# Kernel tuning notes

Hardware: AMD Instinct MI355X
Metric: run time of the kernel (lower is better)

## Reference

```python
import jax, jax.numpy as jnp
import numpy as np

B, REP = 32, 1024
N_VERBS, N_ROLES, N_NOUNS, MR = 504, 190, 11538, 6
HID, NHEADS, MAXN = 32, 4, 512


def setup_inputs() -> dict:
    key = jax.random.key(0)
    ks = jax.random.split(key, 16)
    s = 0.05  # weight scale
    return {
        "rep": jax.random.normal(ks[0], (B, REP), jnp.float32),
        "W_v": jax.random.normal(ks[1], (REP, N_VERBS), jnp.float32) * s,
        "b_v": jax.random.normal(ks[2], (N_VERBS,), jnp.float32) * s,
        "W_r": jax.random.normal(ks[3], (REP, N_ROLES * HID), jnp.float32) * s,
        "b_r": jax.random.normal(ks[4], (N_ROLES * HID,), jnp.float32) * s,
        "attn_in_w": jax.random.normal(ks[5], (3, 3 * HID, HID), jnp.float32) * s,
        "attn_in_b": jax.random.normal(ks[6], (3, 3 * HID), jnp.float32) * s,
        "attn_out_w": jax.random.normal(ks[7], (3, HID, HID), jnp.float32) * s,
        "attn_out_b": jax.random.normal(ks[8], (3, HID), jnp.float32) * s,
        "W_n": jax.random.normal(ks[9], (HID, N_NOUNS), jnp.float32) * s,
        "b_n": jax.random.normal(ks[10], (N_NOUNS,), jnp.float32) * s,
        "r_n_idx": jax.random.randint(ks[11], (N_ROLES, MAXN), 0, N_NOUNS, jnp.int32),
        "pad_v_r": jax.random.randint(ks[12], (N_VERBS, MR), 0, N_ROLES + 1, jnp.int32),
    }


def _mha(x, in_w, in_b, out_w, out_b):
    # x: [L, B, E] self-attention, torch nn.MultiheadAttention semantics
    L, Bn, E = x.shape
    hd = E // NHEADS
    qkv = x @ in_w.T + in_b                      # [L, B, 3E]
    q, k, v = jnp.split(qkv, 3, axis=-1)
    q = q.reshape(L, Bn, NHEADS, hd)
    k = k.reshape(L, Bn, NHEADS, hd)
    v = v.reshape(L, Bn, NHEADS, hd)
    scores = jnp.einsum("lbhd,mbhd->bhlm", q, k) / jnp.sqrt(jnp.float32(hd))
    attn = jax.nn.softmax(scores, axis=-1)
    out = jnp.einsum("bhlm,mbhd->lbhd", attn, v).reshape(L, Bn, E)
    return out @ out_w.T + out_b


def reference(rep, W_v, b_v, W_r, b_r, attn_in_w, attn_in_b, attn_out_w,
              attn_out_b, W_n, b_n, r_n_idx, pad_v_r):
    batch = rep.shape[0]
    v_potential = rep @ W_v + b_v                          # [B, V]
    node = (rep @ W_r + b_r).reshape(batch, N_ROLES, HID)
    node = jnp.transpose(node, (1, 0, 2))                  # [R, B, H]
    for i in range(3):
        node = _mha(node, attn_in_w[i], attn_in_b[i], attn_out_w[i], attn_out_b[i])
    rn_potential = node @ W_n + b_n                        # [R, B, N_nouns]

    # grouped index_select per role: [R, B, MAXN]
    grouped = jax.vmap(lambda pot, idx: pot[:, idx])(rn_potential, r_n_idx)
    r_max = grouped.max(axis=-1)                           # [R, B]
    maxi = grouped.argmax(axis=-1)                         # [R, B]
    rn_marginal = r_max + jnp.log(jnp.exp(grouped - r_max[..., None]).sum(-1))
    r_maxi = jax.vmap(lambda idx, mi: idx[mi])(r_n_idx, maxi)  # global noun ids

    # [B, R] then prepend the zero/padding column -> [B, 1+R]
    zeros_f = jnp.zeros((batch, 1), rn_marginal.dtype)
    zeros_i = jnp.zeros((batch, 1), r_maxi.dtype)
    rn_marginal = jnp.concatenate([zeros_f, rn_marginal.T], axis=1)
    r_max = jnp.concatenate([zeros_f, r_max.T], axis=1)
    r_maxi = jnp.concatenate([zeros_i, r_maxi.T], axis=1)

    # gather per-verb role groups: [B, V, MR]
    vrn_marginal_g = rn_marginal[:, pad_v_r]
    vr_max_g = r_max[:, pad_v_r]
    vr_maxi_g = r_maxi[:, pad_v_r]

    v_marginal = vrn_marginal_g.sum(2) + v_potential       # [B, V]
    m = v_marginal.max(1)
    norm = m + jnp.log(jnp.exp(v_marginal - m[:, None]).sum(1))
    v_max = vr_max_g.sum(2) + v_potential                  # [B, V]
    return (rep, v_potential, rn_potential, norm, v_max, vr_maxi_g)
```

## Files before the change

### kernel.cpp

```cpp
#include <hip/hip_runtime.h>
#include <math.h>

#define B_    32
#define REP_  1024
#define NV_   504
#define NR_   190
#define NN_   11538
#define MR_   6
#define HID_  32
#define NH_   4
#define HD_   8
#define MAXN_ 512

#define O_VP   32768
#define O_RN   48896
#define O_NORM 70199936
#define O_VMAX 70199968
#define O_MAXI 70216096

#define W_REPT  0
#define W_WT    32768
#define W_PN    401984
#define W_PV    1958464
#define W_N0    2087488
#define W_HOB   2282048
#define W_HOA   2476608
#define W_MARG  2671168
#define W_RMAX  2677248
#define W_RMAXI 2683328
#define W_WC    2689408

__global__ __launch_bounds__(256) void k_tr_rep(const float* __restrict__ rep,
                                                float* __restrict__ repT) {
    int gid = blockIdx.x * 256 + threadIdx.x;
    int b = gid & 31, k = gid >> 5;
    repT[gid] = rep[b * REP_ + k];
}

__global__ __launch_bounds__(256) void k_pre(const float* __restrict__ Wn,
                                             float* __restrict__ Wt,
                                             const float* __restrict__ ainw,
                                             const float* __restrict__ ainb,
                                             const float* __restrict__ aoutw,
                                             const float* __restrict__ aoutb,
                                             float* __restrict__ wc) {
    __shared__ float t[32][33];
    int tid = threadIdx.x;
    if (blockIdx.x < 361) {
        int n0 = blockIdx.x * 32;
        #pragma unroll
        for (int p = 0; p < 4; p++) {
            int idx = p * 256 + tid;
            int k = idx >> 5, n = idx & 31;
            int nn = n0 + n;
            t[k][n] = (nn < NN_) ? Wn[(size_t)k * NN_ + nn] : 0.f;
        }
        __syncthreads();
        #pragma unroll
        for (int p = 0; p < 4; p++) {
            int idx = p * 256 + tid;
            int n = idx >> 5, k = idx & 31;
            int nn = n0 + n;
            if (nn < NN_) Wt[nn * 32 + k] = t[k][n];
        }
    } else {
        #pragma unroll 1
        for (int layer = 0; layer < 2; layer++) {
            const float* iw  = ainw + (layer + 1) * 3072;
            const float* ib  = ainb + (layer + 1) * 96;
            const float* ow  = aoutw + layer * 1024;
            const float* obv = aoutb + layer * 32;
            float* W = wc + layer * 3168;
            for (int idx = tid; idx < 3072; idx += 256) {
                int row = idx >> 5, d = idx & 31;
                float s = 0.f;
                #pragma unroll
                for (int e = 0; e < 32; e++) s += iw[row * 32 + e] * ow[e * 32 + d];
                W[idx] = s;
            }
            if (tid < 96) {
                float s = ib[tid];
                #pragma unroll
                for (int e = 0; e < 32; e++) s += iw[tid * 32 + e] * obv[e];
                W[3072 + tid] = s;
            }
        }
    }
}

__global__ __launch_bounds__(256) void k_gemm(const float* __restrict__ Wr,
                                              const float* __restrict__ Wv,
                                              const float4* __restrict__ repT4,
                                              float* __restrict__ pn,
                                              float* __restrict__ pv) {
    int bx = blockIdx.x;
    int lane = threadIdx.x & 63;
    int bg = threadIdx.x >> 6;
    int k0 = blockIdx.y * 128;
    int rbase = k0 * 8 + bg * 2;
    float acc[8] = {0.f,0.f,0.f,0.f,0.f,0.f,0.f,0.f};
    if (bx < 95) {
        int c = bx * 64 + lane;
        const float* w = Wr + (size_t)k0 * 6080 + c;
        #pragma unroll 4
        for (int k = 0; k < 128; k++) {
            float wv = w[(size_t)k * 6080];
            float4 ra = repT4[rbase + k * 8];
            float4 rb = repT4[rbase + k * 8 + 1];
            acc[0] += ra.x * wv; acc[1] += ra.y * wv; acc[2] += ra.z * wv; acc[3] += ra.w * wv;
            acc[4] += rb.x * wv; acc[5] += rb.y * wv; acc[6] += rb.z * wv; acc[7] += rb.w * wv;
        }
        size_t base = (size_t)blockIdx.y * 194560 + (size_t)(bg * 8) * 6080 + c;
        #pragma unroll
        for (int i = 0; i < 8; i++) pn[base + (size_t)i * 6080] = acc[i];
    } else {
        int c = (bx - 95) * 64 + lane;
        if (c >= NV_) return;
        const float* w = Wv + (size_t)k0 * NV_ + c;
        #pragma unroll 4
        for (int k = 0; k < 128; k++) {
            float wv = w[(size_t)k * NV_];
            float4 ra = repT4[rbase + k * 8];
            float4 rb = repT4[rbase + k * 8 + 1];
            acc[0] += ra.x * wv; acc[1] += ra.y * wv; acc[2] += ra.z * wv; acc[3] += ra.w * wv;
            acc[4] += rb.x * wv; acc[5] += rb.y * wv; acc[6] += rb.z * wv; acc[7] += rb.w * wv;
        }
        size_t base = (size_t)blockIdx.y * 16128 + (size_t)(bg * 8) * NV_ + c;
        #pragma unroll
        for (int i = 0; i < 8; i++) pv[base + (size_t)i * NV_] = acc[i];
    }
}

__global__ __launch_bounds__(256) void k_reduce(const float* __restrict__ pn,
                                                const float* __restrict__ pv,
                                                const float* __restrict__ br,
                                                const float* __restrict__ bv,
                                                float* __restrict__ node0,
                                                float* __restrict__ vpot) {
    int bid = blockIdx.x, tid = threadIdx.x;
    if (bid < 760) {
        int gid = bid * 256 + tid;
        int b = gid / 6080, c = gid - b * 6080;
        float s = br[c];
        #pragma unroll
        for (int kz = 0; kz < 8; kz++) s += pn[kz * 194560 + gid];
        node0[(c >> 5) * 1024 + b * 32 + (c & 31)] = s;
    } else {
        int gid = (bid - 760) * 256 + tid;
        int v = gid % NV_;
        float s = bv[v];
        #pragma unroll
        for (int kz = 0; kz < 8; kz++) s += pv[kz * 16128 + gid];
        vpot[gid] = s;
    }
}

__global__ __launch_bounds__(256) void k_attn(const float* __restrict__ xin,
                                              const float* __restrict__ winw,
                                              const float* __restrict__ winb,
                                              float* __restrict__ ho) {
    int b = blockIdx.x >> 2, h = blockIdx.x & 3;
    int tid = threadIdx.x;
    __shared__ __align__(16) float qs[192 * 12];
    __shared__ __align__(16) float ks[192 * 12];
    __shared__ __align__(16) float vs[192 * 12];
    __shared__ __align__(16) float pmS[4 * 192];
    __shared__ __align__(16) float psS[4 * 192];
    __shared__ __align__(16) float poS[4 * 192 * 8];

    if (tid < NR_) {
        const float* xr = xin + tid * 1024 + b * 32;
        float4 xv[8];
        #pragma unroll
        for (int q = 0; q < 8; q++) xv[q] = *(const float4*)(xr + q * 4);
        #pragma unroll 1
        for (int part = 0; part < 3; part++) {
            float* dst = (part == 0) ? qs : (part == 1) ? ks : vs;
            #pragma unroll 1
            for (int jj = 0; jj < 8; jj++) {
                int row = part * 32 + h * 8 + jj;
                const float* wr = winw + row * 32;
                float s = winb[row];
                #pragma unroll
                for (int q = 0; q < 8; q++) {
                    s += xv[q].x * wr[q*4+0] + xv[q].y * wr[q*4+1] +
                         xv[q].z * wr[q*4+2] + xv[q].w * wr[q*4+3];
                }
                dst[tid * 12 + jj] = s;
            }
        }
    }
    __syncthreads();

    int wave = tid >> 6, lane = tid & 63;
    int m0 = wave * 48;
    int m1 = (m0 + 48 < NR_) ? (m0 + 48) : NR_;
    float4 qa[3], qb[3];
    #pragma unroll
    for (int i = 0; i < 3; i++) {
        int l = lane + 64 * i;
        if (l < NR_) {
            qa[i] = *(const float4*)&qs[l * 12];
            qb[i] = *(const float4*)&qs[l * 12 + 4];
        } else {
            qa[i] = make_float4(0.f,0.f,0.f,0.f);
            qb[i] = make_float4(0.f,0.f,0.f,0.f);
        }
    }
    float mM[3] = {-INFINITY, -INFINITY, -INFINITY};
    float sS[3] = {0.f, 0.f, 0.f};
    float o[3][8];
    #pragma unroll
    for (int i = 0; i < 3; i++)
        #pragma unroll
        for (int d = 0; d < 8; d++) o[i][d] = 0.f;
    const float scale = 0.3535533905932738f;
    for (int mm = m0; mm < m1; mm++) {
        float4 ka = *(const float4*)&ks[mm * 12];
        float4 kb = *(const float4*)&ks[mm * 12 + 4];
        float4 va = *(const float4*)&vs[mm * 12];
        float4 vb = *(const float4*)&vs[mm * 12 + 4];
        #pragma unroll
        for (int i = 0; i < 3; i++) {
            float sc = (qa[i].x*ka.x + qa[i].y*ka.y + qa[i].z*ka.z + qa[i].w*ka.w +
                        qb[i].x*kb.x + qb[i].y*kb.y + qb[i].z*kb.z + qb[i].w*kb.w) * scale;
            if (sc > mM[i]) {
                float al = __expf(mM[i] - sc);
                sS[i] = sS[i] * al + 1.f;
                mM[i] = sc;
                o[i][0] = o[i][0]*al + va.x; o[i][1] = o[i][1]*al + va.y;
                o[i][2] = o[i][2]*al + va.z; o[i][3] = o[i][3]*al + va.w;
                o[i][4] = o[i][4]*al + vb.x; o[i][5] = o[i][5]*al + vb.y;
                o[i][6] = o[i][6]*al + vb.z; o[i][7] = o[i][7]*al + vb.w;
            } else {
                float p = __expf(sc - mM[i]);
                sS[i] += p;
                o[i][0] += p*va.x; o[i][1] += p*va.y; o[i][2] += p*va.z; o[i][3] += p*va.w;
                o[i][4] += p*vb.x; o[i][5] += p*vb.y; o[i][6] += p*vb.z; o[i][7] += p*vb.w;
            }
        }
    }
    #pragma unroll
    for (int i = 0; i < 3; i++) {
        int slot = wave * 192 + lane + 64 * i;
        pmS[slot] = mM[i];
        psS[slot] = sS[i];
        *(float4*)&poS[slot * 8]     = make_float4(o[i][0], o[i][1], o[i][2], o[i][3]);
        *(float4*)&poS[slot * 8 + 4] = make_float4(o[i][4], o[i][5], o[i][6], o[i][7]);
    }
    __syncthreads();

    if (tid < NR_) {
        float M = pmS[tid], S = psS[tid];
        float4 oa = *(const float4*)&poS[tid * 8];
        float4 ob = *(const float4*)&poS[tid * 8 + 4];
        #pragma unroll
        for (int w = 1; w < 4; w++) {
            int slot = w * 192 + tid;
            float m2 = pmS[slot], s2 = psS[slot];
            float4 pa = *(const float4*)&poS[slot * 8];
            float4 pb = *(const float4*)&poS[slot * 8 + 4];
            if (m2 > M) {
                float al = __expf(M - m2);
                S = S * al + s2;
                oa.x = oa.x*al + pa.x; oa.y = oa.y*al + pa.y; oa.z = oa.z*al + pa.z; oa.w = oa.w*al + pa.w;
                ob.x = ob.x*al + pb.x; ob.y = ob.y*al + pb.y; ob.z = ob.z*al + pb.z; ob.w = ob.w*al + pb.w;
                M = m2;
            } else {
                float p = __expf(m2 - M);
                S += s2 * p;
                oa.x += p*pa.x; oa.y += p*pa.y; oa.z += p*pa.z; oa.w += p*pa.w;
                ob.x += p*pb.x; ob.y += p*pb.y; ob.z += p*pb.z; ob.w += p*pb.w;
            }
        }
        float inv = 1.f / S;
        float* hp = ho + tid * 1024 + b * 32 + h * 8;
        *(float4*)hp       = make_float4(oa.x*inv, oa.y*inv, oa.z*inv, oa.w*inv);
        *(float4*)(hp + 4) = make_float4(ob.x*inv, ob.y*inv, ob.z*inv, ob.w*inv);
    }
}

__global__ __launch_bounds__(256) void k_big(const float* __restrict__ ho3,
                                             const float* __restrict__ ow3,
                                             const float* __restrict__ ob3,
                                             const float* __restrict__ Wn,
                                             const float* __restrict__ bn,
                                             const float* __restrict__ Wt,
                                             const int* __restrict__ rni,
                                             float* __restrict__ out_rn,
                                             float* __restrict__ marg,
                                             float* __restrict__ rmax,
                                             int* __restrict__ rmaxi) {
    int l = blockIdx.x;
    int tid = threadIdx.x;
    __shared__ float owT[1024];
    __shared__ float As[1024];
    __shared__ float pm[32 * 8], psum[32 * 8];
    __shared__ int   pj[32 * 8];

    for (int i = tid; i < 1024; i += 256) {
        int d = i >> 5, hh = i & 31;
        owT[i] = ow3[hh * 32 + d];
    }

    if (blockIdx.y < 23) {
        int b = tid >> 3, hq = tid & 7;
        float4 hv[8];
        {
            const float4* hp = (const float4*)&ho3[(size_t)l * 1024 + b * 32];
            #pragma unroll
            for (int q = 0; q < 8; q++) hv[q] = hp[q];
        }
        __syncthreads();
        {
            float4 a = *(const float4*)&ob3[hq * 4];
            #pragma unroll
            for (int dq = 0; dq < 8; dq++) {
                float4 h4 = hv[dq];
                float4 w0 = *(const float4*)&owT[(dq*4+0)*32 + hq*4];
                float4 w1 = *(const float4*)&owT[(dq*4+1)*32 + hq*4];
                float4 w2 = *(const float4*)&owT[(dq*4+2)*32 + hq*4];
                float4 w3 = *(const float4*)&owT[(dq*4+3)*32 + hq*4];
                a.x += h4.x*w0.x + h4.y*w1.x + h4.z*w2.x + h4.w*w3.x;
                a.y += h4.x*w0.y + h4.y*w1.y + h4.z*w2.y + h4.w*w3.y;
                a.z += h4.x*w0.z + h4.y*w1.z + h4.z*w2.z + h4.w*w3.z;
                a.w += h4.x*w0.w + h4.y*w1.w + h4.z*w2.w + h4.w*w3.w;
            }
            *(float4*)&As[b * 32 + hq * 4] = a;
        }
        __syncthreads();

        int t0 = l * 32;
        int c0 = blockIdx.y * 512;
        int wave = tid >> 6, lane = tid & 63;
        int r0 = wave * 8;
        int c = c0 + lane * 8;
        int rem = NN_ - c;
        if (rem <= 0) return;
        if (rem >= 8) {
            float acc[8][8];
            #pragma unroll
            for (int r = 0; r < 8; r++)
                #pragma unroll
                for (int q = 0; q < 8; q++) acc[r][q] = 0.f;
            #pragma unroll 1
            for (int g = 0; g < 8; g++) {
                float4 av[8];
                #pragma unroll
                for (int r = 0; r < 8; r++)
                    av[r] = *(const float4*)&As[(r0 + r) * 32 + g * 4];
                #pragma unroll
                for (int kk = 0; kk < 4; kk++) {
                    int k = g * 4 + kk;
                    const float* wp = &Wn[(size_t)k * NN_ + c];
                    float2 w0 = *(const float2*)(wp);
                    float2 w1 = *(const float2*)(wp + 2);
                    float2 w2 = *(const float2*)(wp + 4);
                    float2 w3 = *(const float2*)(wp + 6);
                    #pragma unroll
                    for (int r = 0; r < 8; r++) {
                        float a = ((const float*)&av[r])[kk];
                        acc[r][0] += a * w0.x; acc[r][1] += a * w0.y;
                        acc[r][2] += a * w1.x; acc[r][3] += a * w1.y;
                        acc[r][4] += a * w2.x; acc[r][5] += a * w2.y;
                        acc[r][6] += a * w3.x; acc[r][7] += a * w3.y;
                    }
                }
            }
            float bb[8];
            #pragma unroll
            for (int q = 0; q < 8; q++) bb[q] = bn[c + q];
            #pragma unroll
            for (int r = 0; r < 8; r++) {
                size_t base = (size_t)(t0 + r0 + r) * NN_ + c;
                float v0 = acc[r][0]+bb[0], v1 = acc[r][1]+bb[1];
                float v2 = acc[r][2]+bb[2], v3 = acc[r][3]+bb[3];
                float v4 = acc[r][4]+bb[4], v5 = acc[r][5]+bb[5];
                float v6 = acc[r][6]+bb[6], v7 = acc[r][7]+bb[7];
                if (((r0 + r) & 1) == 0) {
                    *(float4*)&out_rn[base]     = make_float4(v0, v1, v2, v3);
                    *(float4*)&out_rn[base + 4] = make_float4(v4, v5, v6, v7);
                } else {
                    *(float2*)&out_rn[base]     = make_float2(v0, v1);
                    *(float4*)&out_rn[base + 2] = make_float4(v2, v3, v4, v5);
                    *(float2*)&out_rn[base + 6] = make_float2(v6, v7);
                }
            }
        } else {
            for (int e = 0; e < rem; e++) {
                float acc[8] = {0.f,0.f,0.f,0.f,0.f,0.f,0.f,0.f};
                for (int k = 0; k < 32; k++) {
                    float wv = Wn[(size_t)k * NN_ + c + e];
                    #pragma unroll
                    for (int r = 0; r < 8; r++) acc[r] += As[(r0 + r) * 32 + k] * wv;
                }
                float bv2 = bn[c + e];
                #pragma unroll
                for (int r = 0; r < 8; r++)
                    out_rn[(size_t)(t0 + r0 + r) * NN_ + c + e] = acc[r] + bv2;
            }
        }
    } else {
        int jg = tid >> 5, b = tid & 31;
        float4 hv[8];
        {
            const float4* hp = (const float4*)&ho3[(size_t)l * 1024 + b * 32];
            #pragma unroll
            for (int q = 0; q < 8; q++) hv[q] = hp[q];
        }
        __syncthreads();
        float4 nd[8];
        #pragma unroll
        for (int q = 0; q < 8; q++) {
            float4 a = *(const float4*)&ob3[q * 4];
            #pragma unroll
            for (int dq = 0; dq < 8; dq++) {
                float4 h4 = hv[dq];
                float4 w0 = *(const float4*)&owT[(dq*4+0)*32 + q*4];
                float4 w1 = *(const float4*)&owT[(dq*4+1)*32 + q*4];
                float4 w2 = *(const float4*)&owT[(dq*4+2)*32 + q*4];
                float4 w3 = *(const float4*)&owT[(dq*4+3)*32 + q*4];
                a.x += h4.x*w0.x + h4.y*w1.x + h4.z*w2.x + h4.w*w3.x;
                a.y += h4.x*w0.y + h4.y*w1.y + h4.z*w2.y + h4.w*w3.y;
                a.z += h4.x*w0.z + h4.y*w1.z + h4.z*w2.z + h4.w*w3.z;
                a.w += h4.x*w0.w + h4.y*w1.w + h4.z*w2.w + h4.w*w3.w;
            }
            nd[q] = a;
        }
        float lm = -INFINITY, ls = 0.f;
        int jm = 0;
        const int* ip = &rni[l * 512];
        for (int jj = 0; jj < 64; jj++) {
            int j = jg * 64 + jj;
            int idx = ip[j];
            const float4* wr = (const float4*)&Wt[idx * 32];
            float s = bn[idx];
            #pragma unroll
            for (int q = 0; q < 8; q++) {
                float4 w4 = wr[q];
                s += nd[q].x*w4.x + nd[q].y*w4.y + nd[q].z*w4.z + nd[q].w*w4.w;
            }
            if (s > lm) { ls = ls * __expf(lm - s) + 1.f; lm = s; jm = j; }
            else        { ls += __expf(s - lm); }
        }
        pm[b * 8 + jg] = lm; psum[b * 8 + jg] = ls; pj[b * 8 + jg] = jm;
        __syncthreads();
        if (tid < 32) {
            int bb = tid;
            float M = pm[bb * 8], S = psum[bb * 8];
            int J = pj[bb * 8];
            for (int i = 1; i < 8; i++) {
                float m2 = pm[bb * 8 + i], s2 = psum[bb * 8 + i];
                if (m2 > M) { S = S * __expf(M - m2) + s2; M = m2; J = pj[bb * 8 + i]; }
                else        { S += s2 * __expf(m2 - M); }
            }
            int t = l * 32 + bb;
            marg[t]  = M + logf(S);
            rmax[t]  = M;
            rmaxi[t] = ip[J];
        }
    }
}

__global__ __launch_bounds__(256) void k_final(const float* __restrict__ marg,
                                               const float* __restrict__ rmax,
                                               const int* __restrict__ rmaxi,
                                               const int* __restrict__ pad,
                                               const float* __restrict__ vpot,
                                               float* __restrict__ out_norm,
                                               float* __restrict__ out_vmax,
                                               float* __restrict__ out_maxi) {
    int b = blockIdx.x, tid = threadIdx.x;
    __shared__ float me[191], xe[191];
    __shared__ int ie[191];
    __shared__ float vm[NV_];
    __shared__ float rbuf[4];
    if (tid < 191) {
        if (tid == 0) { me[0] = 0.f; xe[0] = 0.f; ie[0] = 0; }
        else {
            int t = (tid - 1) * 32 + b;
            me[tid] = marg[t]; xe[tid] = rmax[t]; ie[tid] = rmaxi[t];
        }
    }
    __syncthreads();
    for (int v = tid; v < NV_; v += 256) {
        float sm = 0.f, sx = 0.f;
        float vp = vpot[b * NV_ + v];
        #pragma unroll
        for (int i = 0; i < 6; i++) {
            int p = pad[v * 6 + i];
            sm += me[p]; sx += xe[p];
            out_maxi[(size_t)(b * NV_ + v) * 6 + i] = (float)ie[p];
        }
        vm[v] = sm + vp;
        out_vmax[b * NV_ + v] = sx + vp;
    }
    __syncthreads();
    float m = -INFINITY;
    for (int v = tid; v < NV_; v += 256) m = fmaxf(m, vm[v]);
    #pragma unroll
    for (int off = 32; off > 0; off >>= 1) m = fmaxf(m, __shfl_xor(m, off));
    if ((tid & 63) == 0) rbuf[tid >> 6] = m;
    __syncthreads();
    float M = fmaxf(fmaxf(rbuf[0], rbuf[1]), fmaxf(rbuf[2], rbuf[3]));
    __syncthreads();
    float s = 0.f;
    for (int v = tid; v < NV_; v += 256) s += __expf(vm[v] - M);
    #pragma unroll
    for (int off = 32; off > 0; off >>= 1) s += __shfl_xor(s, off);
    if ((tid & 63) == 0) rbuf[tid >> 6] = s;
    __syncthreads();
    if (tid == 0) out_norm[b] = M + logf(rbuf[0] + rbuf[1] + rbuf[2] + rbuf[3]);
}

extern "C" void kernel_launch(void* const* d_in, const int* in_sizes, int n_in,
                              void* d_out, int out_size, void* d_ws, size_t ws_size,
                              hipStream_t stream) {
    const float* rep   = (const float*)d_in[0];
    const float* Wv    = (const float*)d_in[1];
    const float* bv    = (const float*)d_in[2];
    const float* Wr    = (const float*)d_in[3];
    const float* br    = (const float*)d_in[4];
    const float* ainw  = (const float*)d_in[5];
    const float* ainb  = (const float*)d_in[6];
    const float* aoutw = (const float*)d_in[7];
    const float* aoutb = (const float*)d_in[8];
    const float* Wn    = (const float*)d_in[9];
    const float* bn    = (const float*)d_in[10];
    const int*   rni   = (const int*)d_in[11];
    const int*   pad   = (const int*)d_in[12];
    float* out = (float*)d_out;
    float* ws  = (float*)d_ws;

    float* repT = ws + W_REPT;
    float* Wt   = ws + W_WT;
    float* pn   = ws + W_PN;
    float* pv   = ws + W_PV;
    float* n0   = ws + W_N0;
    float* hoA  = ws + W_HOA;
    float* hoB  = ws + W_HOB;
    float* marg = ws + W_MARG;
    float* rmx  = ws + W_RMAX;
    int*   rmi  = (int*)(ws + W_RMAXI);
    float* wc   = ws + W_WC;

    hipMemcpyAsync(out, rep, 32768 * sizeof(float), hipMemcpyDeviceToDevice, stream);
    k_tr_rep<<<128, 256, 0, stream>>>(rep, repT);
    k_pre<<<362, 256, 0, stream>>>(Wn, Wt, ainw, ainb, aoutw, aoutb, wc);
    k_gemm<<<dim3(103, 8), 256, 0, stream>>>(Wr, Wv, (const float4*)repT, pn, pv);
    k_reduce<<<823, 256, 0, stream>>>(pn, pv, br, bv, n0, out + O_VP);

    k_attn<<<128, 256, 0, stream>>>(n0,  ainw,      ainb,      hoA);
    k_attn<<<128, 256, 0, stream>>>(hoA, wc,        wc + 3072, hoB);
    k_attn<<<128, 256, 0, stream>>>(hoB, wc + 3168, wc + 6240, hoA);

    k_big<<<dim3(190, 24), 256, 0, stream>>>(hoA, aoutw + 2048, aoutb + 64,
                                             Wn, bn, Wt, rni,
                                             out + O_RN, marg, rmx, rmi);
    k_final<<<32, 256, 0, stream>>>(marg, rmx, rmi, pad, out + O_VP,
                                    out + O_NORM, out + O_VMAX, out + O_MAXI);
}
```

Before: 650.1 us.

## Split noun-GEMM blocks by batch half and use nontemporal stores for rn output

The noun-potential GEMM part of k_big now gives each block 16 batch rows of one role instead of 32. This doubles the grid in x, halves the accumulator registers, and adds a launch_bounds occupancy hint of 4 blocks. The ~280MB rn_potential output is written with nontemporal stores so it bypasses the caches. The reduction blocks (y==23) keep their original indexing and exit early for the extra x range. Each W_n column tile is now read by twice as many blocks, and the small prologue that builds the per-block A tile runs twice as often.

```diff
diff --git a/kernel.cpp b/kernel.cpp
--- a/kernel.cpp
+++ b/kernel.cpp
@@ -29,6 +29,9 @@
 #define W_RMAX  2677248
 #define W_RMAXI 2683328
 #define W_WC    2689408
+
+typedef float vf4 __attribute__((ext_vector_type(4)));
+typedef float vf2 __attribute__((ext_vector_type(2)));
 
 __global__ __launch_bounds__(256) void k_tr_rep(const float* __restrict__ rep,
                                                 float* __restrict__ repT) {
@@ -280,23 +283,23 @@
     }
 }
 
-__global__ __launch_bounds__(256) void k_big(const float* __restrict__ ho3,
-                                             const float* __restrict__ ow3,
-                                             const float* __restrict__ ob3,
-                                             const float* __restrict__ Wn,
-                                             const float* __restrict__ bn,
-                                             const float* __restrict__ Wt,
-                                             const int* __restrict__ rni,
-                                             float* __restrict__ out_rn,
-                                             float* __restrict__ marg,
-                                             float* __restrict__ rmax,
-                                             int* __restrict__ rmaxi) {
-    int l = blockIdx.x;
+__global__ __launch_bounds__(256, 4) void k_big(const float* __restrict__ ho3,
+                                                const float* __restrict__ ow3,
+                                                const float* __restrict__ ob3,
+                                                const float* __restrict__ Wn,
+                                                const float* __restrict__ bn,
+                                                const float* __restrict__ Wt,
+                                                const int* __restrict__ rni,
+                                                float* __restrict__ out_rn,
+                                                float* __restrict__ marg,
+                                                float* __restrict__ rmax,
+                                                int* __restrict__ rmaxi) {
+    if (blockIdx.y == 23 && blockIdx.x >= 190) return;
     int tid = threadIdx.x;
     __shared__ float owT[1024];
-    __shared__ float As[1024];
-    __shared__ float pm[32 * 8], psum[32 * 8];
-    __shared__ int   pj[32 * 8];
+    __shared__ float As[512];
+    __shared__ float pm[256], psum[256];
+    __shared__ int   pj[256];
 
     for (int i = tid; i < 1024; i += 256) {
         int d = i >> 5, hh = i & 31;
@@ -304,15 +307,18 @@
     }
 
     if (blockIdx.y < 23) {
-        int b = tid >> 3, hq = tid & 7;
+        int bx = blockIdx.x;
+        int l  = bx >> 1;
+        int bhalf = (bx & 1) * 16;
         float4 hv[8];
-        {
-            const float4* hp = (const float4*)&ho3[(size_t)l * 1024 + b * 32];
+        int bl = tid >> 3, hq = tid & 7;
+        if (tid < 128) {
+            const float4* hp = (const float4*)&ho3[(size_t)l * 1024 + (bhalf + bl) * 32];
             #pragma unroll
             for (int q = 0; q < 8; q++) hv[q] = hp[q];
         }
         __syncthreads();
-        {
+        if (tid < 128) {
             float4 a = *(const float4*)&ob3[hq * 4];
             #pragma unroll
             for (int dq = 0; dq < 8; dq++) {
@@ -326,28 +332,28 @@
                 a.z += h4.x*w0.z + h4.y*w1.z + h4.z*w2.z + h4.w*w3.z;
                 a.w += h4.x*w0.w + h4.y*w1.w + h4.z*w2.w + h4.w*w3.w;
             }
-            *(float4*)&As[b * 32 + hq * 4] = a;
+            *(float4*)&As[bl * 32 + hq * 4] = a;
         }
         __syncthreads();
 
-        int t0 = l * 32;
+        int t0 = bx * 16;
         int c0 = blockIdx.y * 512;
         int wave = tid >> 6, lane = tid & 63;
-        int r0 = wave * 8;
+        int r0 = wave * 4;
         int c = c0 + lane * 8;
         int rem = NN_ - c;
         if (rem <= 0) return;
         if (rem >= 8) {
-            float acc[8][8];
-            #pragma unroll
-            for (int r = 0; r < 8; r++)
+            float acc[4][8];
+            #pragma unroll
+            for (int r = 0; r < 4; r++)
                 #pragma unroll
                 for (int q = 0; q < 8; q++) acc[r][q] = 0.f;
             #pragma unroll 1
             for (int g = 0; g < 8; g++) {
-                float4 av[8];
-                #pragma unroll
-                for (int r = 0; r < 8; r++)
+                float4 av[4];
+                #pragma unroll
+                for (int r = 0; r < 4; r++)
                     av[r] = *(const float4*)&As[(r0 + r) * 32 + g * 4];
                 #pragma unroll
                 for (int kk = 0; kk < 4; kk++) {
@@ -358,7 +364,7 @@
                     float2 w2 = *(const float2*)(wp + 4);
                     float2 w3 = *(const float2*)(wp + 6);
                     #pragma unroll
-                    for (int r = 0; r < 8; r++) {
+                    for (int r = 0; r < 4; r++) {
                         float a = ((const float*)&av[r])[kk];
                         acc[r][0] += a * w0.x; acc[r][1] += a * w0.y;
                         acc[r][2] += a * w1.x; acc[r][3] += a * w1.y;
@@ -371,36 +377,38 @@
             #pragma unroll
             for (int q = 0; q < 8; q++) bb[q] = bn[c + q];
             #pragma unroll
-            for (int r = 0; r < 8; r++) {
+            for (int r = 0; r < 4; r++) {
                 size_t base = (size_t)(t0 + r0 + r) * NN_ + c;
                 float v0 = acc[r][0]+bb[0], v1 = acc[r][1]+bb[1];
                 float v2 = acc[r][2]+bb[2], v3 = acc[r][3]+bb[3];
                 float v4 = acc[r][4]+bb[4], v5 = acc[r][5]+bb[5];
                 float v6 = acc[r][6]+bb[6], v7 = acc[r][7]+bb[7];
-                if (((r0 + r) & 1) == 0) {
-                    *(float4*)&out_rn[base]     = make_float4(v0, v1, v2, v3);
-                    *(float4*)&out_rn[base + 4] = make_float4(v4, v5, v6, v7);
+                if ((r & 1) == 0) {
+                    __builtin_nontemporal_store((vf4){v0,v1,v2,v3}, (vf4*)&out_rn[base]);
+                    __builtin_nontemporal_store((vf4){v4,v5,v6,v7}, (vf4*)&out_rn[base + 4]);
                 } else {
-                    *(float2*)&out_rn[base]     = make_float2(v0, v1);
-                    *(float4*)&out_rn[base + 2] = make_float4(v2, v3, v4, v5);
-                    *(float2*)&out_rn[base + 6] = make_float2(v6, v7);
+                    __builtin_nontemporal_store((vf2){v0,v1},       (vf2*)&out_rn[base]);
+                    __builtin_nontemporal_store((vf4){v2,v3,v4,v5}, (vf4*)&out_rn[base + 2]);
+                    __builtin_nontemporal_store((vf2){v6,v7},       (vf2*)&out_rn[base + 6]);
                 }
             }
         } else {
             for (int e = 0; e < rem; e++) {
-                float acc[8] = {0.f,0.f,0.f,0.f,0.f,0.f,0.f,0.f};
+                float acc[4] = {0.f,0.f,0.f,0.f};
                 for (int k = 0; k < 32; k++) {
                     float wv = Wn[(size_t)k * NN_ + c + e];
                     #pragma unroll
-                    for (int r = 0; r < 8; r++) acc[r] += As[(r0 + r) * 32 + k] * wv;
+                    for (int r = 0; r < 4; r++) acc[r] += As[(r0 + r) * 32 + k] * wv;
                 }
                 float bv2 = bn[c + e];
                 #pragma unroll
-                for (int r = 0; r < 8; r++)
-                    out_rn[(size_t)(t0 + r0 + r) * NN_ + c + e] = acc[r] + bv2;
+                for (int r = 0; r < 4; r++)
+                    __builtin_nontemporal_store(acc[r] + bv2,
+                        &out_rn[(size_t)(t0 + r0 + r) * NN_ + c + e]);
             }
         }
     } else {
+        int l = blockIdx.x;
         int jg = tid >> 5, b = tid & 31;
         float4 hv[8];
         {
@@ -554,7 +562,7 @@
     k_attn<<<128, 256, 0, stream>>>(hoA, wc,        wc + 3072, hoB);
     k_attn<<<128, 256, 0, stream>>>(hoB, wc + 3168, wc + 6240, hoA);
 
-    k_big<<<dim3(190, 24), 256, 0, stream>>>(hoA, aoutw + 2048, aoutb + 64,
+    k_big<<<dim3(380, 24), 256, 0, stream>>>(hoA, aoutw + 2048, aoutb + 64,
                                              Wn, bn, Wt, rni,
                                              out + O_RN, marg, rmx, rmi);
     k_final<<<32, 256, 0, stream>>>(marg, rmx, rmi, pad, out + O_VP,
```

Measured after the change: 769.4 us. +18.4%, slower.

## Retile noun-potential GEMM with LDS-staged weights and 64x256 output tiles

Applied to the files above, without the earlier changes.

Reorganizes the big rn_potential GEMM in k_big. Each block now stages a 32x256 slice of Wn into shared memory and computes a 64-row by 256-column output tile from a transposed activation tile, instead of reading Wn straight from global memory per 32-row tile. The grid becomes 1D, with the 190 role-reduction blocks placed first, and launch bounds now request 4 blocks per CU. The aim is to cut global Wn traffic and improve occupancy, at the cost of more LDS use per block and a recomputed out-projection per tile.

```diff
diff --git a/kernel.cpp b/kernel.cpp
--- a/kernel.cpp
+++ b/kernel.cpp
@@ -280,31 +280,127 @@
     }
 }
 
-__global__ __launch_bounds__(256) void k_big(const float* __restrict__ ho3,
-                                             const float* __restrict__ ow3,
-                                             const float* __restrict__ ob3,
-                                             const float* __restrict__ Wn,
-                                             const float* __restrict__ bn,
-                                             const float* __restrict__ Wt,
-                                             const int* __restrict__ rni,
-                                             float* __restrict__ out_rn,
-                                             float* __restrict__ marg,
-                                             float* __restrict__ rmax,
-                                             int* __restrict__ rmaxi) {
-    int l = blockIdx.x;
+__global__ __launch_bounds__(256, 4) void k_big(const float* __restrict__ ho3,
+                                                const float* __restrict__ ow3,
+                                                const float* __restrict__ ob3,
+                                                const float* __restrict__ Wn,
+                                                const float* __restrict__ bn,
+                                                const float* __restrict__ Wt,
+                                                const int* __restrict__ rni,
+                                                float* __restrict__ out_rn,
+                                                float* __restrict__ marg,
+                                                float* __restrict__ rmax,
+                                                int* __restrict__ rmaxi) {
+    int bid = blockIdx.x;
     int tid = threadIdx.x;
-    __shared__ float owT[1024];
-    __shared__ float As[1024];
-    __shared__ float pm[32 * 8], psum[32 * 8];
-    __shared__ int   pj[32 * 8];
-
-    for (int i = tid; i < 1024; i += 256) {
-        int d = i >> 5, hh = i & 31;
-        owT[i] = ow3[hh * 32 + d];
-    }
-
-    if (blockIdx.y < 23) {
-        int b = tid >> 3, hq = tid & 7;
+    __shared__ __align__(16) float smem[8192 + 2048 + 1024 + 32];
+    float* Ws  = smem;
+    float* Ask = smem + 8192;
+    float* ows = smem + 10240;
+    float* obs = smem + 11264;
+
+    for (int i = tid; i < 1024; i += 256) ows[i] = ow3[i];
+    if (tid < 32) obs[tid] = ob3[tid];
+
+    if (bid >= 190) {
+        int g  = bid - 190;
+        int bx = g % 95;
+        int by = g / 95;
+        int t0 = bx * 64;
+        int c0 = by * 256;
+        bool tail = (c0 + 256 > NN_);
+
+        #pragma unroll
+        for (int p = 0; p < 16; p++) {
+            int idx = p * 256 + tid;
+            int k  = idx >> 7;
+            int c2 = (idx & 127) * 2;
+            int cg = c0 + c2;
+            float2 v = (cg < NN_) ? *(const float2*)&Wn[(size_t)k * NN_ + cg]
+                                  : make_float2(0.f, 0.f);
+            *(float2*)&Ws[k * 256 + c2] = v;
+        }
+        __syncthreads();
+
+        {
+            int r = tid >> 2, hq = tid & 3;
+            const float4* hp = (const float4*)&ho3[(size_t)(t0 + r) * 32];
+            float4 hv[8];
+            #pragma unroll
+            for (int q = 0; q < 8; q++) hv[q] = hp[q];
+            #pragma unroll
+            for (int i = 0; i < 8; i++) {
+                int h = hq * 8 + i;
+                float s = obs[h];
+                #pragma unroll
+                for (int d4 = 0; d4 < 8; d4++) {
+                    float4 h4 = hv[d4];
+                    float4 w = *(const float4*)&ows[h * 32 + d4 * 4];
+                    s += h4.x*w.x + h4.y*w.y + h4.z*w.z + h4.w*w.w;
+                }
+                Ask[h * 64 + r] = s;
+            }
+        }
+        __syncthreads();
+
+        int wave = tid >> 6, lane = tid & 63;
+        int r0 = wave * 16;
+        int cL = lane * 4;
+        int c  = c0 + cL;
+        float acc[16][4];
+        #pragma unroll
+        for (int r = 0; r < 16; r++)
+            #pragma unroll
+            for (int q = 0; q < 4; q++) acc[r][q] = 0.f;
+
+        #pragma unroll 4
+        for (int k = 0; k < 32; k++) {
+            float4 wv = *(const float4*)&Ws[k * 256 + cL];
+            float4 av[4];
+            av[0] = *(const float4*)&Ask[k * 64 + r0];
+            av[1] = *(const float4*)&Ask[k * 64 + r0 + 4];
+            av[2] = *(const float4*)&Ask[k * 64 + r0 + 8];
+            av[3] = *(const float4*)&Ask[k * 64 + r0 + 12];
+            const float* ap = (const float*)av;
+            #pragma unroll
+            for (int r = 0; r < 16; r++) {
+                float a = ap[r];
+                acc[r][0] += a * wv.x; acc[r][1] += a * wv.y;
+                acc[r][2] += a * wv.z; acc[r][3] += a * wv.w;
+            }
+        }
+
+        if (!tail) {
+            float4 bb = *(const float4*)&bn[c];
+            #pragma unroll
+            for (int r = 0; r < 16; r++) {
+                size_t base = (size_t)(t0 + r0 + r) * NN_ + c;
+                float v0 = acc[r][0] + bb.x, v1 = acc[r][1] + bb.y;
+                float v2 = acc[r][2] + bb.z, v3 = acc[r][3] + bb.w;
+                if ((r & 1) == 0) {
+                    *(float4*)&out_rn[base] = make_float4(v0, v1, v2, v3);
+                } else {
+                    *(float2*)&out_rn[base]     = make_float2(v0, v1);
+                    *(float2*)&out_rn[base + 2] = make_float2(v2, v3);
+                }
+            }
+        } else {
+            #pragma unroll
+            for (int r = 0; r < 16; r++) {
+                size_t base = (size_t)(t0 + r0 + r) * NN_;
+                #pragma unroll
+                for (int q = 0; q < 4; q++) {
+                    if (c + q < NN_)
+                        out_rn[base + c + q] = acc[r][q] + bn[c + q];
+                }
+            }
+        }
+    } else {
+        int l = bid;
+        int jg = tid >> 5, b = tid & 31;
+        float* pm   = smem;
+        float* psum = smem + 256;
+        int*   pj   = (int*)(smem + 512);
         float4 hv[8];
         {
             const float4* hp = (const float4*)&ho3[(size_t)l * 1024 + b * 32];
@@ -312,120 +408,23 @@
             for (int q = 0; q < 8; q++) hv[q] = hp[q];
         }
         __syncthreads();
-        {
-            float4 a = *(const float4*)&ob3[hq * 4];
-            #pragma unroll
-            for (int dq = 0; dq < 8; dq++) {
-                float4 h4 = hv[dq];
-                float4 w0 = *(const float4*)&owT[(dq*4+0)*32 + hq*4];
-                float4 w1 = *(const float4*)&owT[(dq*4+1)*32 + hq*4];
-                float4 w2 = *(const float4*)&owT[(dq*4+2)*32 + hq*4];
-                float4 w3 = *(const float4*)&owT[(dq*4+3)*32 + hq*4];
-                a.x += h4.x*w0.x + h4.y*w1.x + h4.z*w2.x + h4.w*w3.x;
-                a.y += h4.x*w0.y + h4.y*w1.y + h4.z*w2.y + h4.w*w3.y;
-                a.z += h4.x*w0.z + h4.y*w1.z + h4.z*w2.z + h4.w*w3.z;
-                a.w += h4.x*w0.w + h4.y*w1.w + h4.z*w2.w + h4.w*w3.w;
-            }
-            *(float4*)&As[b * 32 + hq * 4] = a;
-        }
-        __syncthreads();
-
-        int t0 = l * 32;
-        int c0 = blockIdx.y * 512;
-        int wave = tid >> 6, lane = tid & 63;
-        int r0 = wave * 8;
-        int c = c0 + lane * 8;
-        int rem = NN_ - c;
-        if (rem <= 0) return;
-        if (rem >= 8) {
-            float acc[8][8];
-            #pragma unroll
-            for (int r = 0; r < 8; r++)
+        float4 nd[8];
+        #pragma unroll
+        for (int q = 0; q < 8; q++) {
+            float s[4];
+            #pragma unroll
+            for (int j = 0; j < 4; j++) {
+                int h = q * 4 + j;
+                float a = obs[h];
                 #pragma unroll
-                for (int q = 0; q < 8; q++) acc[r][q] = 0.f;
-            #pragma unroll 1
-            for (int g = 0; g < 8; g++) {
-                float4 av[8];
-                #pragma unroll
-                for (int r = 0; r < 8; r++)
-                    av[r] = *(const float4*)&As[(r0 + r) * 32 + g * 4];
-                #pragma unroll
-                for (int kk = 0; kk < 4; kk++) {
-                    int k = g * 4 + kk;
-                    const float* wp = &Wn[(size_t)k * NN_ + c];
-                    float2 w0 = *(const float2*)(wp);
-                    float2 w1 = *(const float2*)(wp + 2);
-                    float2 w2 = *(const float2*)(wp + 4);
-                    float2 w3 = *(const float2*)(wp + 6);
-                    #pragma unroll
-                    for (int r = 0; r < 8; r++) {
-                        float a = ((const float*)&av[r])[kk];
-                        acc[r][0] += a * w0.x; acc[r][1] += a * w0.y;
-                        acc[r][2] += a * w1.x; acc[r][3] += a * w1.y;
-                        acc[r][4] += a * w2.x; acc[r][5] += a * w2.y;
-                        acc[r][6] += a * w3.x; acc[r][7] += a * w3.y;
-                    }
+                for (int d4 = 0; d4 < 8; d4++) {
+                    float4 h4 = hv[d4];
+                    float4 w = *(const float4*)&ows[h * 32 + d4 * 4];
+                    a += h4.x*w.x + h4.y*w.y + h4.z*w.z + h4.w*w.w;
                 }
-            }
-            float bb[8];
-            #pragma unroll
-            for (int q = 0; q < 8; q++) bb[q] = bn[c + q];
-            #pragma unroll
-            for (int r = 0; r < 8; r++) {
-                size_t base = (size_t)(t0 + r0 + r) * NN_ + c;
-                float v0 = acc[r][0]+bb[0], v1 = acc[r][1]+bb[1];
-                float v2 = acc[r][2]+bb[2], v3 = acc[r][3]+bb[3];
-                float v4 = acc[r][4]+bb[4], v5 = acc[r][5]+bb[5];
-                float v6 = acc[r][6]+bb[6], v7 = acc[r][7]+bb[7];
-                if (((r0 + r) & 1) == 0) {
-                    *(float4*)&out_rn[base]     = make_float4(v0, v1, v2, v3);
-                    *(float4*)&out_rn[base + 4] = make_float4(v4, v5, v6, v7);
-                } else {
-                    *(float2*)&out_rn[base]     = make_float2(v0, v1);
-                    *(float4*)&out_rn[base + 2] = make_float4(v2, v3, v4, v5);
-                    *(float2*)&out_rn[base + 6] = make_float2(v6, v7);
-                }
-            }
-        } else {
-            for (int e = 0; e < rem; e++) {
-                float acc[8] = {0.f,0.f,0.f,0.f,0.f,0.f,0.f,0.f};
-                for (int k = 0; k < 32; k++) {
-                    float wv = Wn[(size_t)k * NN_ + c + e];
-                    #pragma unroll
-                    for (int r = 0; r < 8; r++) acc[r] += As[(r0 + r) * 32 + k] * wv;
-                }
-                float bv2 = bn[c + e];
-                #pragma unroll
-                for (int r = 0; r < 8; r++)
-                    out_rn[(size_t)(t0 + r0 + r) * NN_ + c + e] = acc[r] + bv2;
-            }
-        }
-    } else {
-        int jg = tid >> 5, b = tid & 31;
-        float4 hv[8];
-        {
-            const float4* hp = (const float4*)&ho3[(size_t)l * 1024 + b * 32];
-            #pragma unroll
-            for (int q = 0; q < 8; q++) hv[q] = hp[q];
-        }
-        __syncthreads();
-        float4 nd[8];
-        #pragma unroll
-        for (int q = 0; q < 8; q++) {
-            float4 a = *(const float4*)&ob3[q * 4];
-            #pragma unroll
-            for (int dq = 0; dq < 8; dq++) {
-                float4 h4 = hv[dq];
-                float4 w0 = *(const float4*)&owT[(dq*4+0)*32 + q*4];
-                float4 w1 = *(const float4*)&owT[(dq*4+1)*32 + q*4];
-                float4 w2 = *(const float4*)&owT[(dq*4+2)*32 + q*4];
-                float4 w3 = *(const float4*)&owT[(dq*4+3)*32 + q*4];
-                a.x += h4.x*w0.x + h4.y*w1.x + h4.z*w2.x + h4.w*w3.x;
-                a.y += h4.x*w0.y + h4.y*w1.y + h4.z*w2.y + h4.w*w3.y;
-                a.z += h4.x*w0.z + h4.y*w1.z + h4.z*w2.z + h4.w*w3.z;
-                a.w += h4.x*w0.w + h4.y*w1.w + h4.z*w2.w + h4.w*w3.w;
-            }
-            nd[q] = a;
+                s[j] = a;
+            }
+            nd[q] = make_float4(s[0], s[1], s[2], s[3]);
         }
         float lm = -INFINITY, ls = 0.f;
         int jm = 0;
@@ -554,7 +553,7 @@
     k_attn<<<128, 256, 0, stream>>>(hoA, wc,        wc + 3072, hoB);
     k_attn<<<128, 256, 0, stream>>>(hoB, wc + 3168, wc + 6240, hoA);
 
-    k_big<<<dim3(190, 24), 256, 0, stream>>>(hoA, aoutw + 2048, aoutb + 64,
+    k_big<<<190 + 95 * 46, 256, 0, stream>>>(hoA, aoutw + 2048, aoutb + 64,
                                              Wn, bn, Wt, rni,
                                              out + O_RN, marg, rmx, rmi);
     k_final<<<32, 256, 0, stream>>>(marg, rmx, rmi, pad, out + O_VP,
```

After: 588.7 us. 9.5% less time.
